# Kernel optimization log

Hardware: AMD Instinct MI355X
Metric: run time of the kernel (lower is better)

The kernel has to match this reference:

```python
import jax, jax.numpy as jnp
import numpy as np

B, S, HID = 2, 2048, 1024
NH, NKV, D = 16, 4, 64
SCALE = 1.0 / np.sqrt(D).astype(np.float32)
SOFTCAP = 30.0
WINDOW = 1024
NEG = -1e30


def setup_inputs() -> dict:
    key = jax.random.key(0)
    kx, kq, kk, kv, ko = jax.random.split(key, 5)
    std = 0.02
    return {
        "x": jax.random.normal(kx, (B, S, HID), jnp.float32),
        "Wq": jax.random.normal(kq, (NH * D, HID), jnp.float32) * std,
        "Wk": jax.random.normal(kk, (NKV * D, HID), jnp.float32) * std,
        "Wv": jax.random.normal(kv, (NKV * D, HID), jnp.float32) * std,
        "Wo": jax.random.normal(ko, (HID, NH * D), jnp.float32) * std,
    }


def reference(x, Wq, Wk, Wv, Wo):
    b, s, _ = x.shape
    n_rep = NH // NKV
    q = (x @ Wq.T).reshape(b, s, NH, D)    # [B,S,NH,D]
    k = (x @ Wk.T).reshape(b, s, NKV, D)   # [B,S,NKV,D]
    v = (x @ Wv.T).reshape(b, s, NKV, D)
    # repeat_kv: each kv head repeated n_rep times consecutively
    k = jnp.repeat(k, n_rep, axis=2)       # [B,S,NH,D]
    v = jnp.repeat(v, n_rep, axis=2)
    scores = jnp.einsum('bqhd,bkhd->bhqk', q, k) * SCALE
    # logit softcapping
    scores = SOFTCAP * jnp.tanh(scores / SOFTCAP)
    # causal + sliding-window mask: keep keys j with i-WINDOW < j <= i
    i = jnp.arange(s)[:, None]
    j = jnp.arange(s)[None, :]
    mask = (j <= i) & (j > i - WINDOW)
    scores = jnp.where(mask, scores, NEG)
    p = jax.nn.softmax(scores, axis=-1)
    o = jnp.einsum('bhqk,bkhd->bqhd', p, v).reshape(b, s, NH * D)
    return o @ Wo.T
```

## Files before the change

kernel.cpp:

```cpp
#include <hip/hip_runtime.h>

typedef __attribute__((ext_vector_type(8))) short bf16x8;
typedef __attribute__((ext_vector_type(4))) short bf16x4;
typedef __attribute__((ext_vector_type(4))) float f32x4;

#define DEVI __device__ __forceinline__

constexpr int Bsz = 2, Ssz = 2048, HID = 1024, NH = 16, NKV = 4, Dh = 64;
constexpr int QKVC = NH * Dh + 2 * NKV * Dh;
constexpr int WINDOW = 1024;
constexpr float SCALE_ = 0.125f;
constexpr float SOFTCAP = 30.0f;
constexpr int TOK = Bsz * Ssz;

DEVI unsigned short f2b(float f) {
  unsigned u = __float_as_uint(f);
  u += 0x7fffu + ((u >> 16) & 1u);
  return (unsigned short)(u >> 16);
}

DEVI void async16(const void* g, void* l) {
  __builtin_amdgcn_global_load_lds(
      (const __attribute__((address_space(1))) unsigned int*)g,
      (__attribute__((address_space(3))) unsigned int*)l, 16, 0, 0);
}

__global__ __launch_bounds__(256) void cvt_all(
    const float* __restrict__ x, const float* __restrict__ wq,
    const float* __restrict__ wk, const float* __restrict__ wv,
    const float* __restrict__ wo, unsigned short* __restrict__ xb,
    unsigned short* __restrict__ wqkv, unsigned short* __restrict__ wob) {
  constexpr int NX = TOK * HID / 4, NQ = NH * Dh * HID / 4,
                NK = NKV * Dh * HID / 4;
  int i = blockIdx.x * 256 + threadIdx.x;
  const float* src;
  unsigned short* dst;
  if (i < NX) { src = x; dst = xb; }
  else if ((i -= NX) < NQ) { src = wq; dst = wqkv; }
  else if ((i -= NQ) < NK) { src = wk; dst = wqkv + NH * Dh * HID; }
  else if ((i -= NK) < NK) { src = wv; dst = wqkv + (NH * Dh + NKV * Dh) * HID; }
  else if ((i -= NK) < NQ) { src = wo; dst = wob; }
  else return;
  float4 v = reinterpret_cast<const float4*>(src)[i];
  ushort4 o2;
  o2.x = f2b(v.x); o2.y = f2b(v.y); o2.z = f2b(v.z); o2.w = f2b(v.w);
  reinterpret_cast<ushort4*>(dst)[i] = o2;
}

template <bool F32OUT>
__global__ __launch_bounds__(256) void gemm_bt(
    const unsigned short* __restrict__ A, const unsigned short* __restrict__ Bt,
    void* __restrict__ Cv, int N) {
  constexpr int K = 1024, BK = 32;
  __shared__ unsigned short As[128 * BK];
  __shared__ unsigned short Bs[128 * BK];
  const int t = threadIdx.x;
  const int lane = t & 63, w = t >> 6;
  const int wr = w >> 1, wc = w & 1;
  const int lq = lane & 15, lg = lane >> 4;
  const long arow0 = (long)blockIdx.x * 128;
  const long bcol0 = (long)blockIdx.y * 128;
  const unsigned short* ag = A + (arow0 + (t >> 2)) * K + (t & 3) * 8;
  const unsigned short* bg = Bt + (bcol0 + (t >> 2)) * K + (t & 3) * 8;
  f32x4 acc[4][4] = {};
  for (int kk = 0; kk < K; kk += BK) {
    __syncthreads();
    async16(ag + kk, &As[t * 8]);
    async16(ag + kk + 64 * K, &As[2048 + t * 8]);
    async16(bg + kk, &Bs[t * 8]);
    async16(bg + kk + 64 * K, &Bs[2048 + t * 8]);
    __syncthreads();
    bf16x8 af[4], bfr[4];
#pragma unroll
    for (int m = 0; m < 4; ++m)
      af[m] = *(const bf16x8*)&As[(wr * 64 + m * 16 + lq) * BK + lg * 8];
#pragma unroll
    for (int n = 0; n < 4; ++n)
      bfr[n] = *(const bf16x8*)&Bs[(wc * 64 + n * 16 + lq) * BK + lg * 8];
#pragma unroll
    for (int m = 0; m < 4; ++m)
#pragma unroll
      for (int n = 0; n < 4; ++n)
        acc[m][n] = __builtin_amdgcn_mfma_f32_16x16x32_bf16(af[m], bfr[n],
                                                            acc[m][n], 0, 0, 0);
  }
#pragma unroll
  for (int m = 0; m < 4; ++m)
#pragma unroll
    for (int n = 0; n < 4; ++n)
#pragma unroll
      for (int r = 0; r < 4; ++r) {
        long row = arow0 + wr * 64 + m * 16 + lg * 4 + r;
        long col = bcol0 + wc * 64 + n * 16 + lq;
        if (F32OUT)
          ((float*)Cv)[row * N + col] = acc[m][n][r];
        else
          ((unsigned short*)Cv)[row * N + col] = f2b(acc[m][n][r]);
      }
}

__global__ __launch_bounds__(256) void attn(
    const unsigned short* __restrict__ qkv, unsigned short* __restrict__ o) {
  constexpr int KB = 64;
  __shared__ unsigned short Ks[KB * Dh];
  __shared__ unsigned short Vsw[KB * Dh];
  __shared__ unsigned short Vt[Dh * KB];
  __shared__ unsigned short Pl[4 * 16 * 64];
  const int t = threadIdx.x, lane = t & 63, w = t >> 6;
  const int lq = lane & 15, lg = lane >> 4;
  const int qt = blockIdx.x, h = blockIdx.y, b = blockIdx.z;
  const int kh = h >> 2;
  const long tokb = (long)b * Ssz;
  const int q0 = qt * 64;
  const int qi = q0 + w * 16 + lq;
  bf16x8 qf[2];
  {
    const unsigned short* qp = qkv + (tokb + qi) * QKVC + h * Dh + lg * 8;
    qf[0] = *(const bf16x8*)qp;
    qf[1] = *(const bf16x8*)(qp + 32);
  }
  float m_run = -1e30f, l_run = 0.f;
  f32x4 oacc[4] = {};
  unsigned short* pw = &Pl[w * 1024];
  int kstart = q0 - WINDOW + 1;
  if (kstart < 0) kstart = 0;
  kstart &= ~(KB - 1);
  for (int k0 = kstart; k0 <= q0; k0 += KB) {
    __syncthreads();
    {
      const unsigned short* kg =
          qkv + (tokb + k0 + (t >> 3)) * QKVC + NH * Dh + kh * Dh +
          (((t & 7) ^ ((t >> 3) & 7)) * 8);
      async16(kg, &Ks[t * 8]);
      async16(kg + 32 * QKVC, &Ks[2048 + t * 8]);
      int vkey = t >> 3, vphys = t & 7;
      const unsigned short* vbase =
          qkv + (tokb + k0) * QKVC + (NH * Dh + NKV * Dh) + kh * Dh;
      async16(vbase + (long)vkey * QKVC + ((vphys ^ (vkey & 7)) * 8),
              &Vsw[t * 8]);
      async16(vbase + (long)(vkey + 32) * QKVC + ((vphys ^ (vkey & 7)) * 8),
              &Vsw[2048 + t * 8]);
    }
    __syncthreads();
#pragma unroll
    for (int pp = 0; pp < 2; ++pp) {
      int dblk = w + pp * 4;
      bf16x8 vv = *(const bf16x8*)&Vsw[lane * 64 + ((dblk ^ (lane & 7)) * 8)];
#pragma unroll
      for (int e = 0; e < 8; ++e) {
        int d = dblk * 8 + e;
        Vt[d * 64 + (((lane >> 3) ^ e) * 8) + (lane & 7)] = (unsigned short)vv[e];
      }
    }
    __syncthreads();
    f32x4 st[4] = {};
#pragma unroll
    for (int kb = 0; kb < 4; ++kb) {
      bf16x8 kf0 =
          *(const bf16x8*)&Ks[(kb * 16 + lq) * Dh + ((lg ^ (lq & 7)) * 8)];
      bf16x8 kf1 = *(const bf16x8*)&Ks[(kb * 16 + lq) * Dh +
                                       (((lg + 4) ^ (lq & 7)) * 8)];
      st[kb] = __builtin_amdgcn_mfma_f32_16x16x32_bf16(kf0, qf[0], st[kb], 0, 0, 0);
      st[kb] = __builtin_amdgcn_mfma_f32_16x16x32_bf16(kf1, qf[1], st[kb], 0, 0, 0);
    }
    float sc[16];
    float pmax = -1e30f;
#pragma unroll
    for (int kb = 0; kb < 4; ++kb)
#pragma unroll
      for (int r = 0; r < 4; ++r) {
        float s = st[kb][r] * SCALE_;
        float e2 = __expf(s * (2.0f / SOFTCAP));
        s = SOFTCAP * (1.0f - 2.0f / (e2 + 1.0f));
        int j = k0 + kb * 16 + lg * 4 + r;
        bool ok = (j <= qi) & (j > qi - WINDOW);
        s = ok ? s : -1e30f;
        sc[kb * 4 + r] = s;
        pmax = fmaxf(pmax, s);
      }
    pmax = fmaxf(pmax, __shfl_xor(pmax, 16));
    pmax = fmaxf(pmax, __shfl_xor(pmax, 32));
    float m_new = fmaxf(m_run, pmax);
    float alpha = __expf(m_run - m_new);
    float psum = 0.f;
    unsigned short pb[16];
#pragma unroll
    for (int ii = 0; ii < 16; ++ii) {
      float p = (sc[ii] > -1e29f) ? __expf(sc[ii] - m_new) : 0.f;
      psum += p;
      pb[ii] = f2b(p);
    }
    psum += __shfl_xor(psum, 16);
    psum += __shfl_xor(psum, 32);
    l_run = l_run * alpha + psum;
    m_run = m_new;
#pragma unroll
    for (int kb = 0; kb < 4; ++kb) {
      bf16x4 pk = {(short)pb[kb * 4], (short)pb[kb * 4 + 1],
                   (short)pb[kb * 4 + 2], (short)pb[kb * 4 + 3]};
      int phys = (kb * 2 + (lg >> 1)) ^ (lq & 7);
      *(bf16x4*)&pw[lq * 64 + phys * 8 + (lg & 1) * 4] = pk;
    }
#pragma unroll
    for (int r = 0; r < 4; ++r) {
      float ar = __uint_as_float((unsigned)__builtin_amdgcn_ds_bpermute(
          (lg * 4 + r) * 4, (int)__float_as_uint(alpha)));
#pragma unroll
      for (int db = 0; db < 4; ++db) oacc[db][r] *= ar;
    }
#pragma unroll
    for (int s2 = 0; s2 < 2; ++s2) {
      bf16x8 pa = *(const bf16x8*)&pw[lq * 64 + (((s2 * 4 + lg) ^ (lq & 7)) * 8)];
#pragma unroll
      for (int db = 0; db < 4; ++db) {
        const int d = db * 16 + lq;
        bf16x8 vb = *(const bf16x8*)&Vt[d * 64 + (((s2 * 4 + lg) ^ (lq & 7)) * 8)];
        oacc[db] = __builtin_amdgcn_mfma_f32_16x16x32_bf16(pa, vb, oacc[db], 0, 0, 0);
      }
    }
  }
#pragma unroll
  for (int r = 0; r < 4; ++r) {
    float lr = __uint_as_float((unsigned)__builtin_amdgcn_ds_bpermute(
        (lg * 4 + r) * 4, (int)__float_as_uint(l_run)));
    float inv = 1.0f / lr;
    long row = tokb + q0 + w * 16 + lg * 4 + r;
#pragma unroll
    for (int db = 0; db < 4; ++db)
      o[row * (NH * Dh) + h * Dh + db * 16 + lq] = f2b(oacc[db][r] * inv);
  }
}

extern "C" void kernel_launch(void* const* d_in, const int* in_sizes, int n_in,
                              void* d_out, int out_size, void* d_ws,
                              size_t ws_size, hipStream_t stream) {
  const float* x = (const float*)d_in[0];
  const float* wq = (const float*)d_in[1];
  const float* wk = (const float*)d_in[2];
  const float* wv = (const float*)d_in[3];
  const float* wo = (const float*)d_in[4];
  char* ws = (char*)d_ws;
  unsigned short* xb = (unsigned short*)(ws);
  unsigned short* ob = (unsigned short*)(ws);
  unsigned short* wqkv = (unsigned short*)(ws + 8l * 1024 * 1024);
  unsigned short* wob = (unsigned short*)(ws + 11l * 1024 * 1024);
  unsigned short* qkvb = (unsigned short*)d_out;
  float* out = (float*)d_out;

  cvt_all<<<6656, 256, 0, stream>>>(x, wq, wk, wv, wo, xb, wqkv, wob);
  gemm_bt<false><<<dim3(TOK / 128, QKVC / 128), 256, 0, stream>>>(xb, wqkv, qkvb, QKVC);
  attn<<<dim3(Ssz / 64, NH, Bsz), 256, 0, stream>>>(qkvb, ob);
  gemm_bt<true><<<dim3(TOK / 128, HID / 128), 256, 0, stream>>>(ob, wob, out, HID);
}
```

Baseline: 220.6 us.

## Pre-transpose V in separate kernel and double-buffer K/V loads in attention

Adds a small kernel that writes V transposed per KV head, so the attention loop loads V directly into its transposed LDS layout instead of doing an in-LDS transpose each tile. K and V tiles are double-buffered, with the next tile's async loads issued before computing the current one, and two of three barriers per iteration are removed. Masking is skipped for tiles fully inside the causal window. This costs an extra launch plus a global write and read of V.

```diff
diff --git a/kernel.cpp b/kernel.cpp
--- a/kernel.cpp
+++ b/kernel.cpp
@@ -99,12 +99,37 @@
       }
 }
 
+__global__ __launch_bounds__(256) void vtrans(
+    const unsigned short* __restrict__ qkv, unsigned short* __restrict__ vT) {
+  __shared__ unsigned short Vsw[64 * 64];
+  const int t = threadIdx.x;
+  const int s0 = blockIdx.x * 64, kh = blockIdx.y, b = blockIdx.z;
+  const unsigned short* vg =
+      qkv + ((long)b * Ssz + s0 + (t >> 3)) * QKVC + (NH * Dh + NKV * Dh) +
+      kh * Dh + (((t & 7) ^ ((t >> 3) & 7)) * 8);
+  async16(vg, &Vsw[t * 8]);
+  async16(vg + 32 * QKVC, &Vsw[2048 + t * 8]);
+  __syncthreads();
+  const int d = t >> 2, sc_ = t & 3;
+  bf16x8 o0, o1;
+#pragma unroll
+  for (int j = 0; j < 8; ++j) {
+    int s = sc_ * 16 + j;
+    o0[j] = (short)Vsw[s * 64 + (((d >> 3) ^ (s & 7)) * 8) + (d & 7)];
+    int s2 = s + 8;
+    o1[j] = (short)Vsw[s2 * 64 + (((d >> 3) ^ (s2 & 7)) * 8) + (d & 7)];
+  }
+  long orow = ((long)(b * NKV + kh) * Dh + d) * Ssz + s0 + sc_ * 16;
+  *(bf16x8*)&vT[orow] = o0;
+  *(bf16x8*)&vT[orow + 8] = o1;
+}
+
 __global__ __launch_bounds__(256) void attn(
-    const unsigned short* __restrict__ qkv, unsigned short* __restrict__ o) {
+    const unsigned short* __restrict__ qkv,
+    const unsigned short* __restrict__ vT, unsigned short* __restrict__ o) {
   constexpr int KB = 64;
-  __shared__ unsigned short Ks[KB * Dh];
-  __shared__ unsigned short Vsw[KB * Dh];
-  __shared__ unsigned short Vt[Dh * KB];
+  __shared__ unsigned short Ks[2][KB * Dh];
+  __shared__ unsigned short Vt[2][Dh * KB];
   __shared__ unsigned short Pl[4 * 16 * 64];
   const int t = threadIdx.x, lane = t & 63, w = t >> 6;
   const int lq = lane & 15, lg = lane >> 4;
@@ -113,82 +138,97 @@
   const long tokb = (long)b * Ssz;
   const int q0 = qt * 64;
   const int qi = q0 + w * 16 + lq;
+  const int qlo = q0 + w * 16;
   bf16x8 qf[2];
   {
     const unsigned short* qp = qkv + (tokb + qi) * QKVC + h * Dh + lg * 8;
     qf[0] = *(const bf16x8*)qp;
     qf[1] = *(const bf16x8*)(qp + 32);
   }
+  const unsigned short* kg0 = qkv + (tokb + (t >> 3)) * QKVC + NH * Dh +
+                              kh * Dh + (((t & 7) ^ ((t >> 3) & 7)) * 8);
+  const unsigned short* vg0 = vT + ((long)(b * NKV + kh) * Dh + (t >> 3)) * Ssz +
+                              (((t & 7) ^ ((t >> 3) & 7)) * 8);
   float m_run = -1e30f, l_run = 0.f;
   f32x4 oacc[4] = {};
   unsigned short* pw = &Pl[w * 1024];
   int kstart = q0 - WINDOW + 1;
   if (kstart < 0) kstart = 0;
   kstart &= ~(KB - 1);
+
+#define STAGE(buf, kk)                                    \
+  do {                                                    \
+    async16(kg0 + (long)(kk)*QKVC, &Ks[buf][t * 8]);      \
+    async16(kg0 + (long)((kk) + 32) * QKVC,               \
+            &Ks[buf][2048 + t * 8]);                      \
+    async16(vg0 + (kk), &Vt[buf][t * 8]);                 \
+    async16(vg0 + (kk) + 32 * Ssz, &Vt[buf][2048 + t * 8]); \
+  } while (0)
+
+  STAGE(0, kstart);
+  __syncthreads();
+  int cur = 0;
   for (int k0 = kstart; k0 <= q0; k0 += KB) {
-    __syncthreads();
-    {
-      const unsigned short* kg =
-          qkv + (tokb + k0 + (t >> 3)) * QKVC + NH * Dh + kh * Dh +
-          (((t & 7) ^ ((t >> 3) & 7)) * 8);
-      async16(kg, &Ks[t * 8]);
-      async16(kg + 32 * QKVC, &Ks[2048 + t * 8]);
-      int vkey = t >> 3, vphys = t & 7;
-      const unsigned short* vbase =
-          qkv + (tokb + k0) * QKVC + (NH * Dh + NKV * Dh) + kh * Dh;
-      async16(vbase + (long)vkey * QKVC + ((vphys ^ (vkey & 7)) * 8),
-              &Vsw[t * 8]);
-      async16(vbase + (long)(vkey + 32) * QKVC + ((vphys ^ (vkey & 7)) * 8),
-              &Vsw[2048 + t * 8]);
-    }
-    __syncthreads();
-#pragma unroll
-    for (int pp = 0; pp < 2; ++pp) {
-      int dblk = w + pp * 4;
-      bf16x8 vv = *(const bf16x8*)&Vsw[lane * 64 + ((dblk ^ (lane & 7)) * 8)];
-#pragma unroll
-      for (int e = 0; e < 8; ++e) {
-        int d = dblk * 8 + e;
-        Vt[d * 64 + (((lane >> 3) ^ e) * 8) + (lane & 7)] = (unsigned short)vv[e];
-      }
-    }
-    __syncthreads();
+    if (k0 + KB <= q0) STAGE(cur ^ 1, k0 + KB);
     f32x4 st[4] = {};
 #pragma unroll
     for (int kb = 0; kb < 4; ++kb) {
-      bf16x8 kf0 =
-          *(const bf16x8*)&Ks[(kb * 16 + lq) * Dh + ((lg ^ (lq & 7)) * 8)];
-      bf16x8 kf1 = *(const bf16x8*)&Ks[(kb * 16 + lq) * Dh +
-                                       (((lg + 4) ^ (lq & 7)) * 8)];
+      bf16x8 kf0 = *(const bf16x8*)&Ks[cur][(kb * 16 + lq) * Dh +
+                                           ((lg ^ (lq & 7)) * 8)];
+      bf16x8 kf1 = *(const bf16x8*)&Ks[cur][(kb * 16 + lq) * Dh +
+                                            (((lg + 4) ^ (lq & 7)) * 8)];
       st[kb] = __builtin_amdgcn_mfma_f32_16x16x32_bf16(kf0, qf[0], st[kb], 0, 0, 0);
       st[kb] = __builtin_amdgcn_mfma_f32_16x16x32_bf16(kf1, qf[1], st[kb], 0, 0, 0);
     }
+    const bool need_mask = (k0 + KB - 1 > qlo) | (k0 <= qlo + 15 - WINDOW);
     float sc[16];
     float pmax = -1e30f;
-#pragma unroll
-    for (int kb = 0; kb < 4; ++kb)
-#pragma unroll
-      for (int r = 0; r < 4; ++r) {
-        float s = st[kb][r] * SCALE_;
-        float e2 = __expf(s * (2.0f / SOFTCAP));
-        s = SOFTCAP * (1.0f - 2.0f / (e2 + 1.0f));
-        int j = k0 + kb * 16 + lg * 4 + r;
-        bool ok = (j <= qi) & (j > qi - WINDOW);
-        s = ok ? s : -1e30f;
-        sc[kb * 4 + r] = s;
-        pmax = fmaxf(pmax, s);
-      }
+    if (need_mask) {
+#pragma unroll
+      for (int kb = 0; kb < 4; ++kb)
+#pragma unroll
+        for (int r = 0; r < 4; ++r) {
+          float s = st[kb][r] * SCALE_;
+          float e2 = __expf(s * (2.0f / SOFTCAP));
+          s = SOFTCAP * (1.0f - 2.0f / (e2 + 1.0f));
+          int j = k0 + kb * 16 + lg * 4 + r;
+          bool ok = (j <= qi) & (j > qi - WINDOW);
+          s = ok ? s : -1e30f;
+          sc[kb * 4 + r] = s;
+          pmax = fmaxf(pmax, s);
+        }
+    } else {
+#pragma unroll
+      for (int kb = 0; kb < 4; ++kb)
+#pragma unroll
+        for (int r = 0; r < 4; ++r) {
+          float s = st[kb][r] * SCALE_;
+          float e2 = __expf(s * (2.0f / SOFTCAP));
+          s = SOFTCAP * (1.0f - 2.0f / (e2 + 1.0f));
+          sc[kb * 4 + r] = s;
+          pmax = fmaxf(pmax, s);
+        }
+    }
     pmax = fmaxf(pmax, __shfl_xor(pmax, 16));
     pmax = fmaxf(pmax, __shfl_xor(pmax, 32));
     float m_new = fmaxf(m_run, pmax);
     float alpha = __expf(m_run - m_new);
     float psum = 0.f;
     unsigned short pb[16];
-#pragma unroll
-    for (int ii = 0; ii < 16; ++ii) {
-      float p = (sc[ii] > -1e29f) ? __expf(sc[ii] - m_new) : 0.f;
-      psum += p;
-      pb[ii] = f2b(p);
+    if (need_mask) {
+#pragma unroll
+      for (int ii = 0; ii < 16; ++ii) {
+        float p = (sc[ii] > -1e29f) ? __expf(sc[ii] - m_new) : 0.f;
+        psum += p;
+        pb[ii] = f2b(p);
+      }
+    } else {
+#pragma unroll
+      for (int ii = 0; ii < 16; ++ii) {
+        float p = __expf(sc[ii] - m_new);
+        psum += p;
+        pb[ii] = f2b(p);
+      }
     }
     psum += __shfl_xor(psum, 16);
     psum += __shfl_xor(psum, 32);
@@ -214,11 +254,15 @@
 #pragma unroll
       for (int db = 0; db < 4; ++db) {
         const int d = db * 16 + lq;
-        bf16x8 vb = *(const bf16x8*)&Vt[d * 64 + (((s2 * 4 + lg) ^ (lq & 7)) * 8)];
+        bf16x8 vb = *(const bf16x8*)&Vt[cur][d * 64 +
+                                            (((s2 * 4 + lg) ^ (lq & 7)) * 8)];
         oacc[db] = __builtin_amdgcn_mfma_f32_16x16x32_bf16(pa, vb, oacc[db], 0, 0, 0);
       }
     }
-  }
+    __syncthreads();
+    cur ^= 1;
+  }
+#undef STAGE
 #pragma unroll
   for (int r = 0; r < 4; ++r) {
     float lr = __uint_as_float((unsigned)__builtin_amdgcn_ds_bpermute(
@@ -245,10 +289,13 @@
   unsigned short* wqkv = (unsigned short*)(ws + 8l * 1024 * 1024);
   unsigned short* wob = (unsigned short*)(ws + 11l * 1024 * 1024);
   unsigned short* qkvb = (unsigned short*)d_out;
+  unsigned short* vT =
+      (unsigned short*)((char*)d_out + 12l * 1024 * 1024);
   float* out = (float*)d_out;
 
   cvt_all<<<6656, 256, 0, stream>>>(x, wq, wk, wv, wo, xb, wqkv, wob);
   gemm_bt<false><<<dim3(TOK / 128, QKVC / 128), 256, 0, stream>>>(xb, wqkv, qkvb, QKVC);
-  attn<<<dim3(Ssz / 64, NH, Bsz), 256, 0, stream>>>(qkvb, ob);
+  vtrans<<<dim3(Ssz / 64, NKV, Bsz), 256, 0, stream>>>(qkvb, vT);
+  attn<<<dim3(Ssz / 64, NH, Bsz), 256, 0, stream>>>(qkvb, vT, ob);
   gemm_bt<true><<<dim3(TOK / 128, HID / 128), 256, 0, stream>>>(ob, wob, out, HID);
 }
```

Result: faster. 210.9 us (-4.4%).
